# Kernel tuning notes

Measured on AMD Instinct MI355X. Metric: run time of the kernel, lower is better.

Reference implementation:

```python
import jax, jax.numpy as jnp
import numpy as np
import math

EMBED_DIM = 256
SEQ_LEN = 4096
BATCH = 4
NUM_SCALES = (24.0, 720.0)


def setup_inputs() -> dict:
    key = jax.random.key(0)
    ks = jax.random.split(key, 8)
    d = EMBED_DIM
    x = jax.random.normal(ks[0], (BATCH, SEQ_LEN, d), dtype=jnp.float32)
    # nn.Linear params: weight [out, in], bias [out]
    s = 1.0 / math.sqrt(d)
    Wq = jax.random.uniform(ks[1], (d, d), jnp.float32, -s, s)
    bq = jax.random.uniform(ks[2], (d,), jnp.float32, -s, s)
    Wk = jax.random.uniform(ks[3], (d, d), jnp.float32, -s, s)
    bk = jax.random.uniform(ks[4], (d,), jnp.float32, -s, s)
    Wv = jax.random.uniform(ks[5], (d, d), jnp.float32, -s, s)
    bv = jax.random.uniform(ks[6], (d,), jnp.float32, -s, s)
    beta = jnp.ones((len(NUM_SCALES),), dtype=jnp.float32)
    return {"x": x, "Wq": Wq, "bq": bq, "Wk": Wk, "bk": bk, "Wv": Wv, "bv": bv, "beta": beta}


def reference(x, Wq, bq, Wk, bk, Wv, bv, beta):
    d = x.shape[-1]
    seq_len = x.shape[1]
    sqrt_d = jnp.asarray(math.sqrt(d), x.dtype)
    # Linear: y = x @ W^T + b
    Q = jnp.einsum('bsd,ed->bse', x, Wq) + bq
    K = jnp.einsum('bsd,ed->bse', x, Wk) + bk
    V = jnp.einsum('bsd,ed->bse', x, Wv) + bv
    attn = jnp.einsum('bse,bte->bst', Q, K) / sqrt_d  # [B,S,S]
    # multi-scale periodic bias (batch-independent): sum_n beta[n]*cos(2*pi*|i-j|/T_n)
    idx = jnp.arange(seq_len, dtype=jnp.float32)
    absdiff = jnp.abs(idx[:, None] - idx[None, :])  # [S,S]
    two_pi = jnp.asarray(2.0 * math.pi, jnp.float32)
    bias = jnp.zeros((seq_len, seq_len), dtype=jnp.float32)
    for n, T in enumerate(NUM_SCALES):
        bias = bias + beta[n] * jnp.cos(two_pi * absdiff / T)
    scores = jax.nn.softmax(attn + bias[None, :, :], axis=-1)
    return jnp.einsum('bst,bte->bse', scores, V)
```

## Files before the change

kernel.cpp:

```cpp
#include <hip/hip_runtime.h>
#include <math.h>
#include <stdint.h>

#define DEV static __device__ __forceinline__
typedef unsigned short u16;

constexpr int D = 256;
constexpr int S = 4096;
constexpr int QSTR = 272;
constexpr int KT_TILE = 8960;
constexpr int VT_TILE = 10240;

typedef short bf16x8 __attribute__((ext_vector_type(8)));
typedef float f32x16 __attribute__((ext_vector_type(16)));
typedef int v2i __attribute__((ext_vector_type(2)));

DEV u16 f2bf(float f){ __bf16 b = (__bf16)f; return __builtin_bit_cast(u16, b); }
DEV float bf2f(u16 h){ return __uint_as_float(((unsigned)h)<<16); }
DEV int packbf(float lo, float hi){ return (int)((((unsigned)f2bf(hi)) << 16) | (unsigned)f2bf(lo)); }
DEV float bfsum2(int d){
  return __uint_as_float(((unsigned)d)<<16) + __uint_as_float(((unsigned)d) & 0xffff0000u);
}
DEV float ex2(float x){ return __builtin_amdgcn_exp2f(x); }
DEV void gl_lds16(const u16* g, u16* l) {
  __builtin_amdgcn_global_load_lds(
      (const __attribute__((address_space(1))) unsigned int*)g,
      (__attribute__((address_space(3))) unsigned int*)l, 16, 0, 0);
}

DEV size_t cm_addr(int rowblock, int chunk, int row_in, int j) {
  return ((size_t)rowblock*4 + chunk)*8192 + (size_t)(((row_in<<3) + j) ^ (row_in & 7))*8;
}
DEV const u16* swz(const u16* base, int row, int slot) {
  return base + ((((row<<3) + slot) ^ (row & 7)) << 3);
}

DEV void softmax_pf(const f32x16& s, int h, float& l_acc, bf16x8* pf) {
  #pragma unroll
  for (int s2 = 0; s2 < 2; ++s2) {
    float e0 = ex2(s[8*s2+0]), e1 = ex2(s[8*s2+1]);
    float e2 = ex2(s[8*s2+2]), e3 = ex2(s[8*s2+3]);
    float e4 = ex2(s[8*s2+4]), e5 = ex2(s[8*s2+5]);
    float e6 = ex2(s[8*s2+6]), e7 = ex2(s[8*s2+7]);
    int P0d0 = packbf(e0, e1), P0d1 = packbf(e2, e3);
    int P1d0 = packbf(e4, e5), P1d1 = packbf(e6, e7);
    l_acc += bfsum2(P0d0) + bfsum2(P0d1) + bfsum2(P1d0) + bfsum2(P1d1);
    v2i w0 = __builtin_amdgcn_permlane32_swap(P0d0, P1d0, false, false);
    v2i w1 = __builtin_amdgcn_permlane32_swap(P0d1, P1d1, false, false);
    int r0 = h ? w0.x : w0.y;
    int r1 = h ? w1.x : w1.y;
    union { int d[4]; bf16x8 v; } u;
    u.d[0] = h ? r0 : P0d0;
    u.d[1] = h ? r1 : P0d1;
    u.d[2] = h ? P1d0 : r0;
    u.d[3] = h ? P1d1 : r1;
    pf[s2] = u.v;
  }
}

__global__ __launch_bounds__(256) void msp_prep(
    const float* __restrict__ x, const float* __restrict__ Wq,
    const float* __restrict__ Wk, const float* __restrict__ Wv,
    const float* __restrict__ beta,
    u16* __restrict__ xc, u16* __restrict__ Wc,
    u16* __restrict__ Qb, u16* __restrict__ Kt,
    float* __restrict__ Lacc)
{
  const int blk = blockIdx.x, tid = threadIdx.x;
  if (blk < 2048) {
    int row = blk*8 + (tid>>5);
    int col = (tid&31)*8;
    const float* p = x + (size_t)row*256 + col;
    union { u16 s[8]; uint4 v; } hh;
    #pragma unroll
    for (int i=0;i<8;++i){ hh.s[i] = f2bf(p[i]); }
    int rb = row >> 7, rin = row & 127;
    int ch = col >> 6, j = (col >> 3) & 7;
    *(uint4*)(xc + cm_addr(rb, ch, rin, j)) = hh.v;
  } else if (blk < 2144) {
    int q = blk - 2048;
    int mat = q >> 5;
    int idx = (q & 31)*2048 + tid*8;
    int o = idx >> 8, cc = idx & 255;
    const float* W = mat==0 ? Wq : (mat==1 ? Wk : Wv);
    float sc = (mat==0) ? 0.09016844005556021f : 1.0f;
    const float* p = W + (size_t)o*256 + cc;
    union { u16 s[8]; uint4 v; } hh;
    #pragma unroll
    for (int i=0;i<8;++i){ hh.s[i] = f2bf(p[i]*sc); }
    int rowg = mat*256 + o;
    int rb = rowg >> 7, rin = rowg & 127;
    int ch = cc >> 6, j = (cc >> 3) & 7;
    *(uint4*)(Wc + cm_addr(rb, ch, rin, j)) = hh.v;
  } else if (blk < 2208) {
    int row = (blk - 2144)*256 + tid;
    int s = row & (S-1);
    int bb = row >> 12;
    constexpr float L2E = 1.4426950408889634f;
    float b0 = beta[0]*L2E, b1 = beta[1]*L2E;
    int i24 = s % 24, i720 = s % 720;
    float t0 = (float)i24  * 0.26179938779914944f;
    float t1 = (float)i720 * 0.008726646259971648f;
    float c0 = cosf(t0), s0 = sinf(t0), c1 = cosf(t1), s1 = sinf(t1);
    float qv[4] = {b0*c0, b0*s0, b1*c1, b1*s1};
    float kv[4] = {c0, s0, c1, s1};
    u16* qp = Qb + (size_t)row*QSTR + 256;
    u16* kp = Kt + (size_t)(bb*128 + (s>>5))*KT_TILE + (s&31)*280 + 256;
    #pragma unroll
    for (int n=0;n<4;++n){
      u16 uh = f2bf(qv[n]); u16 ul = f2bf(qv[n]-bf2f(uh));
      u16 vh = f2bf(kv[n]); u16 vl = f2bf(kv[n]-bf2f(vh));
      qp[n*3+0]=uh; qp[n*3+1]=uh; qp[n*3+2]=ul;
      kp[n*3+0]=vh; kp[n*3+1]=vl; kp[n*3+2]=vh;
    }
    #pragma unroll
    for (int c=12;c<16;++c){ qp[c]=0; kp[c]=0; }
  } else {
    float4* p = (float4*)Lacc;
    float4 z = {0.f,0.f,0.f,0.f};
    #pragma unroll
    for (int c=0;c<16;++c) p[tid + c*256] = z;
  }
}

__global__ __launch_bounds__(256, 2) void msp_proj(
    const u16* __restrict__ xc, const u16* __restrict__ Wc,
    const float* __restrict__ bq, const float* __restrict__ bk, const float* __restrict__ bv,
    u16* __restrict__ Qb, u16* __restrict__ Kt, u16* __restrict__ Vt)
{
  __shared__ __align__(16) u16 smem[2][2][128][64];

  const int tid = threadIdx.x;
  const int w = tid >> 6, lane = tid & 63;
  const int l31 = lane & 31, h = lane >> 5;
  const int m0 = blockIdx.x * 128;
  const int nblk = blockIdx.y;
  const int mat = nblk >> 1, cb = (nblk & 1) * 128;
  const int mh = (w & 1) * 64, nh = (w >> 1) * 64;

  const u16* Ag = xc + (size_t)blockIdx.x*4*8192;
  const u16* Bg = Wc + (size_t)nblk*4*8192;

  {
    #pragma unroll
    for (int i = w; i < 16; i += 4) gl_lds16(Ag + i*512 + lane*8, &smem[0][0][0][0] + i*512);
    #pragma unroll
    for (int i = w; i < 16; i += 4) gl_lds16(Bg + i*512 + lane*8, &smem[0][1][0][0] + i*512);
  }

  f32x16 acc[2][2];
  #pragma unroll
  for (int a=0;a<2;++a)
    #pragma unroll
    for (int c=0;c<2;++c)
      #pragma unroll
      for (int i=0;i<16;++i) acc[a][c][i] = 0.f;

  for (int kc8 = 0; kc8 < 4; ++kc8) {
    __syncthreads();
    const int p = kc8 & 1;
    if (kc8 < 3) {
      const u16* a2 = Ag + (size_t)(kc8+1)*8192;
      const u16* b2 = Bg + (size_t)(kc8+1)*8192;
      #pragma unroll
      for (int i = w; i < 16; i += 4) gl_lds16(a2 + i*512 + lane*8, &smem[p^1][0][0][0] + i*512);
      #pragma unroll
      for (int i = w; i < 16; i += 4) gl_lds16(b2 + i*512 + lane*8, &smem[p^1][1][0][0] + i*512);
    }
    const u16* As = &smem[p][0][0][0];
    const u16* Bs = &smem[p][1][0][0];
    #pragma unroll
    for (int kf = 0; kf < 4; ++kf) {
      const int slot = kf*2 + h;
      bf16x8 a0 = *(const bf16x8*)swz(As, mh + l31, slot);
      bf16x8 a1 = *(const bf16x8*)swz(As, mh + 32 + l31, slot);
      bf16x8 b0 = *(const bf16x8*)swz(Bs, nh + l31, slot);
      bf16x8 b1 = *(const bf16x8*)swz(Bs, nh + 32 + l31, slot);
      acc[0][0] = __builtin_amdgcn_mfma_f32_32x32x16_bf16(a0, b0, acc[0][0], 0,0,0);
      acc[0][1] = __builtin_amdgcn_mfma_f32_32x32x16_bf16(a0, b1, acc[0][1], 0,0,0);
      acc[1][0] = __builtin_amdgcn_mfma_f32_32x32x16_bf16(a1, b0, acc[1][0], 0,0,0);
      acc[1][1] = __builtin_amdgcn_mfma_f32_32x32x16_bf16(a1, b1, acc[1][1], 0,0,0);
    }
  }

  const float* bias = mat==0 ? bq : (mat==1 ? bk : bv);
  const float bsc = (mat==0) ? 0.09016844005556021f : 1.0f;
  float bb_[2];
  #pragma unroll
  for (int ntl=0; ntl<2; ++ntl) bb_[ntl] = bias[cb + nh + ntl*32 + l31] * bsc;

  if (mat <= 1) {
    #pragma unroll
    for (int mt=0; mt<2; ++mt)
      #pragma unroll
      for (int ntl=0; ntl<2; ++ntl)
        #pragma unroll
        for (int r=0; r<16; ++r) {
          int gm = m0 + mh + mt*32 + (r&3) + 8*(r>>2) + 4*h;
          int col = cb + nh + ntl*32 + l31;
          u16 val = f2bf(acc[mt][ntl][r] + bb_[ntl]);
          if (mat == 0) {
            Qb[(size_t)gm*QSTR + col] = val;
          } else {
            int bb2 = gm >> 12, s = gm & (S-1);
            Kt[(size_t)(bb2*128 + (s>>5))*KT_TILE + (s&31)*280 + col] = val;
          }
        }
  } else {
    __syncthreads();
    u16* T = (u16*)smem;
    #pragma unroll
    for (int mt=0; mt<2; ++mt)
      #pragma unroll
      for (int ntl=0; ntl<2; ++ntl)
        #pragma unroll
        for (int r=0; r<16; ++r) {
          int e_loc = nh + ntl*32 + l31;
          int m_loc = mh + mt*32 + (r&3) + 8*(r>>2) + 4*h;
          T[(size_t)e_loc*136 + m_loc] = f2bf(acc[mt][ntl][r] + bb_[ntl]);
        }
    __syncthreads();
    int e_loc = tid >> 1, shalf = (tid & 1)*64;
    int e = cb + e_loc;
    #pragma unroll
    for (int g2 = 0; g2 < 2; ++g2) {
      int gm = m0 + shalf + g2*32;
      int bb2 = gm >> 12, s = gm & (S-1);
      u16* dst = Vt + (size_t)(bb2*128 + (s>>5))*VT_TILE + (size_t)e*40;
      const u16* src = T + (size_t)e_loc*136 + shalf + g2*32;
      #pragma unroll
      for (int k2=0;k2<4;++k2) *(uint4*)(dst + k2*8) = *(const uint4*)(src + k2*8);
    }
  }
}

__global__ __launch_bounds__(512, 2) void msp_attn(
    const u16* __restrict__ Qb, const u16* __restrict__ Kt,
    const u16* __restrict__ Vt, float* __restrict__ out,
    float* __restrict__ P1, float* __restrict__ P23,
    float* __restrict__ Lacc)
{
  __shared__ __align__(16) unsigned char smem[77824];

  const int tid = threadIdx.x;
  const int w = tid >> 6, lane = tid & 63;
  const int l31 = lane & 31, h = lane >> 5;

  const int xg = blockIdx.x;
  const int xcd = xg & 7, j = xg >> 3;
  const int c = xcd*2 + (j & 1);
  const int qt = j >> 1;
  const int b = c >> 2, tq = c & 3;
  const int q0 = qt * 256;
  const int qw = q0 + w*32;

  bf16x8 qf[17];
  {
    const u16* qp = Qb + ((size_t)b*S + qw + l31)*QSTR + h*8;
    #pragma unroll
    for (int s2=0; s2<17; ++s2) qf[s2] = *(const bf16x8*)(qp + s2*16);
  }

  const int tIdx0 = b*128 + tq*32;

  f32x16 oacc[8];
  #pragma unroll
  for (int e=0;e<8;++e)
    #pragma unroll
    for (int i=0;i<16;++i) oacc[e][i] = 0.f;
  float l_acc = 0.f;

  {
    const u16* kg = Kt + (size_t)tIdx0*KT_TILE;
    u16* kl = (u16*)smem;
    #pragma unroll
    for (int i = w; i < 18; i += 8) gl_lds16(kg + i*512 + lane*8, kl + i*512);
  }

  bf16x8 pf[2];

  {
    __syncthreads();
    const u16* kg = Kt + (size_t)(tIdx0 + 1)*KT_TILE;
    u16* kl = (u16*)(smem + 18432);
    #pragma unroll
    for (int i = w; i < 18; i += 8) gl_lds16(kg + i*512 + lane*8, kl + i*512);
    const u16* vg = Vt + (size_t)tIdx0*VT_TILE;
    u16* vl = (u16*)(smem + 36864);
    #pragma unroll
    for (int i = w; i < 20; i += 8) gl_lds16(vg + i*512 + lane*8, vl + i*512);

    const u16* Kp = (const u16*)smem + (size_t)l31*280 + h*8;
    f32x16 sa;
    #pragma unroll
    for (int i=0;i<16;++i) sa[i] = 0.f;
    __builtin_amdgcn_s_setprio(1);
    #pragma unroll
    for (int s2 = 0; s2 < 17; ++s2) {
      bf16x8 kf = *(const bf16x8*)(Kp + s2*16);
      sa = __builtin_amdgcn_mfma_f32_32x32x16_bf16(kf, qf[s2], sa, 0,0,0);
    }
    __builtin_amdgcn_s_setprio(0);
    softmax_pf(sa, h, l_acc, pf);
  }

  for (int it = 1; it < 32; ++it) {
    const int p = it & 1;
    __syncthreads();

    if (it < 31) {
      const u16* kg = Kt + (size_t)(tIdx0 + it + 1)*KT_TILE;
      u16* kl = (u16*)(smem + (p^1)*18432);
      #pragma unroll
      for (int i = w; i < 18; i += 8) gl_lds16(kg + i*512 + lane*8, kl + i*512);
    }
    {
      const u16* vg = Vt + (size_t)(tIdx0 + it)*VT_TILE;
      u16* vl = (u16*)(smem + 36864 + p*20480);
      #pragma unroll
      for (int i = w; i < 20; i += 8) gl_lds16(vg + i*512 + lane*8, vl + i*512);
    }

    const u16* Kp = (const u16*)(smem + p*18432) + (size_t)l31*280 + h*8;
    const u16* Vp = (const u16*)(smem + 36864 + (p^1)*20480) + (size_t)l31*40 + h*8;
    f32x16 sa;
    #pragma unroll
    for (int i=0;i<16;++i) sa[i] = 0.f;
    __builtin_amdgcn_s_setprio(1);
    #pragma unroll
    for (int s2 = 0; s2 < 17; ++s2) {
      bf16x8 kf = *(const bf16x8*)(Kp + s2*16);
      sa = __builtin_amdgcn_mfma_f32_32x32x16_bf16(kf, qf[s2], sa, 0,0,0);
      if (s2 < 16) {
        const u16* vb = Vp + (s2>>1)*(32*40) + (s2&1)*16;
        oacc[s2>>1] = __builtin_amdgcn_mfma_f32_32x32x16_bf16(*(const bf16x8*)vb, pf[s2&1], oacc[s2>>1], 0,0,0);
      }
    }
    __builtin_amdgcn_s_setprio(0);

    softmax_pf(sa, h, l_acc, pf);
  }

  float l_tot = l_acc + __shfl_xor(l_acc, 32, 64);
  if (h == 0) unsafeAtomicAdd(&Lacc[(size_t)b*S + qw + l31], l_tot);

  __syncthreads();
  {
    const u16* Vp = (const u16*)(smem + 36864 + 20480) + (size_t)l31*40 + h*8;
    __builtin_amdgcn_s_setprio(1);
    #pragma unroll
    for (int et = 0; et < 8; ++et) {
      const u16* vb = Vp + et*32*40;
      oacc[et] = __builtin_amdgcn_mfma_f32_32x32x16_bf16(*(const bf16x8*)(vb),      pf[0], oacc[et], 0,0,0);
      oacc[et] = __builtin_amdgcn_mfma_f32_32x32x16_bf16(*(const bf16x8*)(vb + 16), pf[1], oacc[et], 0,0,0);
    }
    __builtin_amdgcn_s_setprio(0);
  }

  float* dst = (tq == 0) ? (out + (size_t)b*S*D)
             : (tq == 1) ? (P1 + (size_t)b*S*D)
                         : (P23 + ((size_t)(tq-2)*4 + b)*S*D);
  float* OflA = (float*)smem;
  float* OflB = (float*)smem + 8320;
  for (int rr = 0; rr < 4; ++rr) {
    __syncthreads();
    if ((w >> 1) == rr) {
      float* Of = (w & 1) ? OflB : OflA;
      #pragma unroll
      for (int et=0; et<8; ++et)
        #pragma unroll
        for (int g=0; g<4; ++g) {
          float4 v4 = { oacc[et][4*g+0], oacc[et][4*g+1], oacc[et][4*g+2], oacc[et][4*g+3] };
          *(float4*)&Of[(size_t)l31*260 + et*32 + 8*g + 4*h] = v4;
        }
    }
    __syncthreads();
    #pragma unroll
    for (int hf = 0; hf < 2; ++hf) {
      const float* Of = hf ? OflB : OflA;
      float* obase = dst + (size_t)(q0 + rr*64 + hf*32)*D;
      #pragma unroll
      for (int q2 = 0; q2 < 4; ++q2) {
        int q = q2*8 + (tid>>6);
        int e4 = (tid & 63)*4;
        *(float4*)(obase + (size_t)q*D + e4) = *(const float4*)&Of[(size_t)q*260 + e4];
      }
    }
  }
}

__global__ __launch_bounds__(256) void msp_norm(
    float* __restrict__ out, const float* __restrict__ P1,
    const float* __restrict__ P23, const float* __restrict__ L)
{
  constexpr size_t PSZ = (size_t)4*S*D;
  int idx = blockIdx.x*256 + threadIdx.x;
  int row = idx >> 6, e0 = (idx & 63)*4;
  size_t off = (size_t)row*256 + e0;
  float inv = 1.0f / L[row];
  float4 v  = *(const float4*)(out + off);
  float4 a  = *(const float4*)(P1  + off);
  float4 b2 = *(const float4*)(P23 + off);
  float4 c2 = *(const float4*)(P23 + PSZ + off);
  v.x = (v.x + a.x + b2.x + c2.x) * inv;
  v.y = (v.y + a.y + b2.y + c2.y) * inv;
  v.z = (v.z + a.z + b2.z + c2.z) * inv;
  v.w = (v.w + a.w + b2.w + c2.w) * inv;
  *(float4*)(out + off) = v;
}

extern "C" void kernel_launch(void* const* d_in, const int* in_sizes, int n_in,
                              void* d_out, int out_size, void* d_ws, size_t ws_size,
                              hipStream_t stream) {
  const float* x    = (const float*)d_in[0];
  const float* Wq   = (const float*)d_in[1];
  const float* bq   = (const float*)d_in[2];
  const float* Wk   = (const float*)d_in[3];
  const float* bk   = (const float*)d_in[4];
  const float* Wv   = (const float*)d_in[5];
  const float* bv   = (const float*)d_in[6];
  const float* beta = (const float*)d_in[7];
  float* out = (float*)d_out;

  char* w = (char*)d_ws;
  u16* xc = (u16*)w;
  float* P1 = (float*)w;
  w += (size_t)16384*512*2;
  u16* Wc = (u16*)w;  w += (size_t)768*512*2;
  u16* Qb = (u16*)w;  w += (size_t)16384*QSTR*2;
  u16* Kt = (u16*)w;  w += (size_t)512*KT_TILE*2;
  u16* Vt = (u16*)w;  w += (size_t)512*VT_TILE*2;
  float* Lacc = (float*)w; w += (size_t)16384*4;
  float* P23 = (float*)w;

  msp_prep<<<2209, 256, 0, stream>>>(x, Wq, Wk, Wv, beta, xc, Wc, Qb, Kt, Lacc);
  msp_proj<<<dim3(128, 6), 256, 0, stream>>>(xc, Wc, bq, bk, bv, Qb, Kt, Vt);
  msp_attn<<<256, 512, 0, stream>>>(Qb, Kt, Vt, out, P1, P23, Lacc);
  msp_norm<<<4096, 256, 0, stream>>>(out, P1, P23, Lacc);
}
```

Measured before the change: 180.9 us.

## Triple-buffer K tiles with partial vmcnt waits to deepen prefetch

Grows LDS and moves K tiles from a double buffer to a triple buffer, prefetching K two iterations ahead. The full __syncthreads at the top of each iteration is replaced by a per-wave partial s_waitcnt vmcnt plus a raw barrier at the end, so only older loads must land. The aim is to hide more global-load latency behind the MFMA work. The larger LDS footprint (96KB per block) may limit how many blocks fit per CU under launch_bounds(512,2), and the hand-counted vmcnt values depend on exact load counts per wave.

```diff
diff --git a/kernel.cpp b/kernel.cpp
--- a/kernel.cpp
+++ b/kernel.cpp
@@ -240,7 +240,7 @@
     float* __restrict__ P1, float* __restrict__ P23,
     float* __restrict__ Lacc)
 {
-  __shared__ __align__(16) unsigned char smem[77824];
+  __shared__ __align__(16) unsigned char smem[96256];
 
   const int tid = threadIdx.x;
   const int w = tid >> 6, lane = tid & 63;
@@ -271,24 +271,28 @@
   float l_acc = 0.f;
 
   {
-    const u16* kg = Kt + (size_t)tIdx0*KT_TILE;
-    u16* kl = (u16*)smem;
+    const u16* kg0 = Kt + (size_t)tIdx0*KT_TILE;
+    u16* kl0 = (u16*)smem;
+    #pragma unroll
+    for (int i = w; i < 18; i += 8) gl_lds16(kg0 + i*512 + lane*8, kl0 + i*512);
+    const u16* kg1 = Kt + (size_t)(tIdx0 + 1)*KT_TILE;
+    u16* kl1 = (u16*)(smem + 18432);
+    #pragma unroll
+    for (int i = w; i < 18; i += 8) gl_lds16(kg1 + i*512 + lane*8, kl1 + i*512);
+  }
+  __syncthreads();
+
+  bf16x8 pf[2];
+
+  {
+    const u16* vg = Vt + (size_t)tIdx0*VT_TILE;
+    u16* vl = (u16*)(smem + 55296);
+    #pragma unroll
+    for (int i = w; i < 20; i += 8) gl_lds16(vg + i*512 + lane*8, vl + i*512);
+    const u16* kg = Kt + (size_t)(tIdx0 + 2)*KT_TILE;
+    u16* kl = (u16*)(smem + 2*18432);
     #pragma unroll
     for (int i = w; i < 18; i += 8) gl_lds16(kg + i*512 + lane*8, kl + i*512);
-  }
-
-  bf16x8 pf[2];
-
-  {
-    __syncthreads();
-    const u16* kg = Kt + (size_t)(tIdx0 + 1)*KT_TILE;
-    u16* kl = (u16*)(smem + 18432);
-    #pragma unroll
-    for (int i = w; i < 18; i += 8) gl_lds16(kg + i*512 + lane*8, kl + i*512);
-    const u16* vg = Vt + (size_t)tIdx0*VT_TILE;
-    u16* vl = (u16*)(smem + 36864);
-    #pragma unroll
-    for (int i = w; i < 20; i += 8) gl_lds16(vg + i*512 + lane*8, vl + i*512);
 
     const u16* Kp = (const u16*)smem + (size_t)l31*280 + h*8;
     f32x16 sa;
@@ -302,27 +306,29 @@
     }
     __builtin_amdgcn_s_setprio(0);
     softmax_pf(sa, h, l_acc, pf);
+
+    if (w < 2) asm volatile("s_waitcnt vmcnt(3)" ::: "memory");
+    else       asm volatile("s_waitcnt vmcnt(2)" ::: "memory");
+    __builtin_amdgcn_s_barrier();
+    asm volatile("" ::: "memory");
   }
 
   for (int it = 1; it < 32; ++it) {
-    const int p = it & 1;
-    __syncthreads();
-
-    if (it < 31) {
-      const u16* kg = Kt + (size_t)(tIdx0 + it + 1)*KT_TILE;
-      u16* kl = (u16*)(smem + (p^1)*18432);
-      #pragma unroll
-      for (int i = w; i < 18; i += 8) gl_lds16(kg + i*512 + lane*8, kl + i*512);
-    }
     {
       const u16* vg = Vt + (size_t)(tIdx0 + it)*VT_TILE;
-      u16* vl = (u16*)(smem + 36864 + p*20480);
+      u16* vl = (u16*)(smem + 55296 + (size_t)(it & 1)*20480);
       #pragma unroll
       for (int i = w; i < 20; i += 8) gl_lds16(vg + i*512 + lane*8, vl + i*512);
     }
-
-    const u16* Kp = (const u16*)(smem + p*18432) + (size_t)l31*280 + h*8;
-    const u16* Vp = (const u16*)(smem + 36864 + (p^1)*20480) + (size_t)l31*40 + h*8;
+    if (it <= 29) {
+      const u16* kg = Kt + (size_t)(tIdx0 + it + 2)*KT_TILE;
+      u16* kl = (u16*)(smem + (size_t)((it + 2) % 3)*18432);
+      #pragma unroll
+      for (int i = w; i < 18; i += 8) gl_lds16(kg + i*512 + lane*8, kl + i*512);
+    }
+
+    const u16* Kp = (const u16*)(smem + (size_t)(it % 3)*18432) + (size_t)l31*280 + h*8;
+    const u16* Vp = (const u16*)(smem + 55296 + (size_t)((it - 1) & 1)*20480) + (size_t)l31*40 + h*8;
     f32x16 sa;
     #pragma unroll
     for (int i=0;i<16;++i) sa[i] = 0.f;
@@ -339,6 +345,17 @@
     __builtin_amdgcn_s_setprio(0);
 
     softmax_pf(sa, h, l_acc, pf);
+
+    if (it <= 29) {
+      if (w < 2) asm volatile("s_waitcnt vmcnt(3)" ::: "memory");
+      else       asm volatile("s_waitcnt vmcnt(2)" ::: "memory");
+    } else if (it == 30) {
+      asm volatile("s_waitcnt vmcnt(0)" ::: "memory");
+    }
+    if (it < 31) {
+      __builtin_amdgcn_s_barrier();
+      asm volatile("" ::: "memory");
+    }
   }
 
   float l_tot = l_acc + __shfl_xor(l_acc, 32, 64);
@@ -346,7 +363,7 @@
 
   __syncthreads();
   {
-    const u16* Vp = (const u16*)(smem + 36864 + 20480) + (size_t)l31*40 + h*8;
+    const u16* Vp = (const u16*)(smem + 55296 + 20480) + (size_t)l31*40 + h*8;
     __builtin_amdgcn_s_setprio(1);
     #pragma unroll
     for (int et = 0; et < 8; ++et) {
```

After: 183.5 us. No clear change (+1.4%).
